# Kernel optimization log

Measured on AMD Instinct MI355X. Metric: run time of the kernel, lower is better.

The kernel has to match this reference:

```python
import jax, jax.numpy as jnp
import numpy as np

# ViT-Base config
C, H, W = 3, 224, 224
NP = 14            # n_patches per side
PS = 16            # patch size (H // NP)
IN_D = C * PS * PS # 768
D = 768            # hidden_d
NH = 12            # n_heads
DH = D // NH       # 64
L = 12             # n_blocks
MLP = 4 * D        # mlp_ratio * hidden_d
OUT = 1000         # out_d
B = 64             # batch
S = NP * NP + 1    # 197 tokens (cls + patches)
EPS = 1e-5


def _pos_embed(seq_len, d):
    # get_positional_embeddings: sin on even dims, cos on odd dims
    i = jnp.arange(seq_len, dtype=jnp.float32)[:, None]
    j = jnp.arange(d, dtype=jnp.float32)[None, :]
    angle = i / jnp.power(10000.0, (j - j % 2) / d)
    return jnp.where(j % 2 == 0, jnp.sin(angle), jnp.cos(angle))


def _ln(x, g, b):
    m = x.mean(-1, keepdims=True)
    v = ((x - m) ** 2).mean(-1, keepdims=True)
    return (x - m) * jax.lax.rsqrt(v + EPS) * g + b


def _attn(x, qkv_w, qkv_b, out_w, out_b):
    n, s, _ = x.shape
    qkv = (x @ qkv_w + qkv_b).reshape(n, s, NH, 3, DH)  # matches torch chunk layout
    q, k, v = qkv[..., 0, :], qkv[..., 1, :], qkv[..., 2, :]
    scores = jnp.einsum('bqhd,bkhd->bhqk', q, k) / (DH ** 0.5)
    w = jax.nn.softmax(scores, axis=-1)
    o = jnp.einsum('bhqk,bkhd->bqhd', w, v).reshape(n, s, D)
    return o @ out_w + out_b


def setup_inputs() -> dict:
    key = jax.random.key(0)
    ks = jax.random.split(key, 16)
    sd = 0.02
    return {
        'images': jax.random.normal(ks[0], (B, C, H, W), jnp.float32),
        'lm_w': jax.random.normal(ks[1], (IN_D, D), jnp.float32) * sd,
        'lm_b': jnp.zeros((D,), jnp.float32),
        'cls_tok': jax.random.uniform(ks[2], (1, D), jnp.float32),
        'ln1_g': jnp.ones((L, D), jnp.float32),
        'ln1_b': jnp.zeros((L, D), jnp.float32),
        'qkv_w': jax.random.normal(ks[3], (L, D, 3 * D), jnp.float32) * sd,
        'qkv_b': jnp.zeros((L, 3 * D), jnp.float32),
        'out_w': jax.random.normal(ks[4], (L, D, D), jnp.float32) * sd,
        'out_b': jnp.zeros((L, D), jnp.float32),
        'ln2_g': jnp.ones((L, D), jnp.float32),
        'ln2_b': jnp.zeros((L, D), jnp.float32),
        'mlp1_w': jax.random.normal(ks[5], (L, D, MLP), jnp.float32) * sd,
        'mlp1_b': jnp.zeros((L, MLP), jnp.float32),
        'mlp2_w': jax.random.normal(ks[6], (L, MLP, D), jnp.float32) * sd,
        'mlp2_b': jnp.zeros((L, D), jnp.float32),
        'head_w': jax.random.normal(ks[7], (D, OUT), jnp.float32) * sd,
        'head_b': jnp.zeros((OUT,), jnp.float32),
    }


def reference(images, lm_w, lm_b, cls_tok, ln1_g, ln1_b, qkv_w, qkv_b,
              out_w, out_b, ln2_g, ln2_b, mlp1_w, mlp1_b, mlp2_w, mlp2_b,
              head_w, head_b):
    n = images.shape[0]
    # patchify: (N,C,H,W) -> (N, NP*NP, C*PS*PS), per-patch flatten order (C, ph, pw)
    p = images.reshape(n, C, NP, PS, NP, PS).transpose(0, 2, 4, 1, 3, 5)
    p = p.reshape(n, NP * NP, IN_D)
    tok = p @ lm_w + lm_b                                   # (N, 196, D)
    cls = jnp.broadcast_to(cls_tok, (n, 1, D))
    x = jnp.concatenate([cls, tok], axis=1) + _pos_embed(S, D)
    for l in range(L):
        x = x + _attn(_ln(x, ln1_g[l], ln1_b[l]), qkv_w[l], qkv_b[l], out_w[l], out_b[l])
        h = _ln(x, ln2_g[l], ln2_b[l])
        x = x + (jax.nn.gelu(h @ mlp1_w[l] + mlp1_b[l], approximate=False) @ mlp2_w[l] + mlp2_b[l])
    return jax.nn.softmax(x[:, 0] @ head_w + head_b, axis=-1)
```

## Files before the change

### kernel.cpp

```cpp
#include <hip/hip_runtime.h>
#include <hip/hip_bf16.h>
#include <math.h>

#define WS_B 64
#define WS_S 197
#define WS_D 768
#define WS_NH 12
#define WS_L 12
#define WS_MLP 3072
#define WS_OUT 1000
#define WS_IND 768
#define WS_NPAT 196
#define SP 208
#define JP 224

typedef __attribute__((ext_vector_type(8))) short bf16x8;
typedef __attribute__((ext_vector_type(4))) float f32x4;

static __device__ __forceinline__ float bf2f(short s) {
    unsigned u = ((unsigned)(unsigned short)s) << 16;
    return __builtin_bit_cast(float, u);
}
static __device__ __forceinline__ short f2bf(float f) {
    unsigned u = __builtin_bit_cast(unsigned, f);
    u = (u + 0x7FFF + ((u >> 16) & 1)) >> 16;
    return (short)u;
}

__global__ __launch_bounds__(256) void wconv_kernel(
    const float* __restrict__ W, short* __restrict__ Wh, int K, int N)
{
    int idx = blockIdx.x * 256 + threadIdx.x;
    int total = (K >> 3) * N;
    if (idx >= total) return;
    int n = idx % N, k8 = idx / N, k0 = k8 << 3;
    short hi[8];
#pragma unroll
    for (int j = 0; j < 8; ++j) hi[j] = f2bf(W[(size_t)(k0 + j) * N + n]);
    *(bf16x8*)(Wh + (size_t)n * K + k0) = *(bf16x8*)hi;
}

__global__ __launch_bounds__(256) void mfma_gemm(
    const short* __restrict__ A, int lda,
    const short* __restrict__ Bh,
    const float* __restrict__ bias, const float* __restrict__ res,
    float* __restrict__ outF, short* __restrict__ outH, int ldc,
    int M, int N, int K, int act)
{
    __shared__ short As[128 * 64];
    __shared__ short Bs[128 * 64];

    const int tid = threadIdx.x;
    const int w = tid >> 6, lane = tid & 63;
    const int bm = blockIdx.y * 128, bn = blockIdx.x * 128;
    const int wm = (w >> 1) * 64, wn = (w & 1) * 64;
    const int lr = lane & 15, lq = lane >> 4;

    f32x4 acc[4][4];
#pragma unroll
    for (int i = 0; i < 4; ++i)
#pragma unroll
        for (int j = 0; j < 4; ++j) acc[i][j] = (f32x4){0.f, 0.f, 0.f, 0.f};

    int aoff[2][4], boff[2][4];
#pragma unroll
    for (int ks = 0; ks < 2; ++ks)
#pragma unroll
        for (int f = 0; f < 4; ++f) {
            int r = wm + f * 16 + lr;
            aoff[ks][f] = r * 64 + (((ks * 4 + lq) ^ (lr & 7)) << 3);
            int rn = wn + f * 16 + lr;
            boff[ks][f] = rn * 64 + (((ks * 4 + lq) ^ (lr & 7)) << 3);
        }

    int srow[4], scs[4];
#pragma unroll
    for (int i = 0; i < 4; ++i) {
        int chunk = w * 64 + i * 256 + lane;
        int row = chunk >> 3, c = chunk & 7;
        srow[i] = row;
        scs[i] = c ^ (row & 7);
    }

    for (int k0 = 0; k0 < K; k0 += 64) {
#pragma unroll
        for (int i = 0; i < 4; ++i) {
            int ldsbase = (w * 64 + i * 256) * 8;
            int arow = bm + srow[i]; if (arow >= M) arow = M - 1;
            const short* ga = A + (size_t)arow * lda + k0 + scs[i] * 8;
            __builtin_amdgcn_global_load_lds(
                (const __attribute__((address_space(1))) void*)ga,
                (__attribute__((address_space(3))) void*)(As + ldsbase), 16, 0, 0);
            const short* gh = Bh + (size_t)(bn + srow[i]) * K + k0 + scs[i] * 8;
            __builtin_amdgcn_global_load_lds(
                (const __attribute__((address_space(1))) void*)gh,
                (__attribute__((address_space(3))) void*)(Bs + ldsbase), 16, 0, 0);
        }
        asm volatile("s_waitcnt vmcnt(0)" ::: "memory");
        __syncthreads();

#pragma unroll
        for (int ks = 0; ks < 2; ++ks) {
            bf16x8 av[4], bv[4];
#pragma unroll
            for (int f = 0; f < 4; ++f) av[f] = *(const bf16x8*)&As[aoff[ks][f]];
#pragma unroll
            for (int f = 0; f < 4; ++f) bv[f] = *(const bf16x8*)&Bs[boff[ks][f]];
#pragma unroll
            for (int fm = 0; fm < 4; ++fm)
#pragma unroll
                for (int fn = 0; fn < 4; ++fn)
                    acc[fm][fn] = __builtin_amdgcn_mfma_f32_16x16x32_bf16(
                        av[fm], bv[fn], acc[fm][fn], 0, 0, 0);
        }
        __syncthreads();
    }

#pragma unroll
    for (int fm = 0; fm < 4; ++fm)
#pragma unroll
        for (int fn = 0; fn < 4; ++fn) {
            int gc = bn + wn + fn * 16 + lr;
            float bvs = bias ? bias[gc] : 0.f;
            int grb = bm + wm + fm * 16 + lq * 4;
#pragma unroll
            for (int r = 0; r < 4; ++r) {
                int gr = grb + r;
                if (gr >= M) continue;
                float v = acc[fm][fn][r] + bvs;
                if (act == 1) v = 0.5f * v * (1.f + erff(v * 0.70710678118654752440f));
                if (res) v += res[(size_t)gr * ldc + gc];
                if (outF) outF[(size_t)gr * ldc + gc] = v;
                else      outH[(size_t)gr * ldc + gc] = f2bf(v);
            }
        }
}

__global__ __launch_bounds__(256) void attn_kernel(
    const short* __restrict__ qkv, short* __restrict__ o)
{
    __shared__ short Qs[SP * 64];
    __shared__ short Ks[SP * 64];
    __shared__ short Vt[64 * 256];
    __shared__ short Ps[4][16 * 256];

    const int bh = blockIdx.x;
    const int n = bh / WS_NH, h = bh % WS_NH;
    const short* base = qkv + (size_t)n * WS_S * 2304 + h * 192;
    const int tid = threadIdx.x;
    const int w = tid >> 6, lane = tid & 63;
    const int lr = lane & 15, lq = lane >> 4;

    const bf16x8 z8 = {0, 0, 0, 0, 0, 0, 0, 0};
    for (int i = lane; i < 512; i += 64) *(bf16x8*)&Ps[w][i * 8] = z8;

    for (int u = tid; u < SP * 8; u += 256) {
        int row = u >> 3, c = u & 7;
        int cs = c ^ (row & 7);
        bf16x8 vq = z8, vk = z8;
        if (row < WS_S) {
            const short* rp = base + (size_t)row * 2304;
            vq = *(const bf16x8*)(rp + cs * 8);
            vk = *(const bf16x8*)(rp + 64 + cs * 8);
        }
        *(bf16x8*)&Qs[row * 64 + c * 8] = vq;
        *(bf16x8*)&Ks[row * 64 + c * 8] = vk;
    }

    for (int u = tid; u < 64 * (JP / 2); u += 256) {
        int d = u & 63, jp = u >> 6;
        int j = jp * 2;
        unsigned val = 0;
        if (j < WS_S) {
            unsigned lo = (unsigned short)base[(size_t)j * 2304 + 128 + d];
            unsigned hi = (j + 1 < WS_S) ? (unsigned short)base[(size_t)(j + 1) * 2304 + 128 + d] : 0u;
            val = lo | (hi << 16);
        }
        int cj = j >> 3, e = j & 7;
        *(unsigned*)&Vt[d * 256 + ((cj ^ (d & 7)) << 3) + e] = val;
    }
    __syncthreads();

    for (int qt = w; qt < 13; qt += 4) {
        bf16x8 qv[2];
#pragma unroll
        for (int ks = 0; ks < 2; ++ks)
            qv[ks] = *(const bf16x8*)&Qs[(qt * 16 + lr) * 64 + (((ks * 4 + lq) ^ (lr & 7)) << 3)];
        f32x4 acc[13];
#pragma unroll
        for (int jt = 0; jt < 13; ++jt) acc[jt] = (f32x4){0.f, 0.f, 0.f, 0.f};
#pragma unroll
        for (int jt = 0; jt < 13; ++jt)
#pragma unroll
            for (int ks = 0; ks < 2; ++ks) {
                bf16x8 kv = *(const bf16x8*)&Ks[(jt * 16 + lr) * 64 + (((ks * 4 + lq) ^ (lr & 7)) << 3)];
                acc[jt] = __builtin_amdgcn_mfma_f32_16x16x32_bf16(kv, qv[ks], acc[jt], 0, 0, 0);
            }

        float s[13][4];
        float m = -1e30f;
#pragma unroll
        for (int jt = 0; jt < 13; ++jt)
#pragma unroll
            for (int r = 0; r < 4; ++r) {
                int j = jt * 16 + lq * 4 + r;
                float v = acc[jt][r] * 0.125f;
                s[jt][r] = v;
                if (j < WS_S) m = fmaxf(m, v);
            }
        m = fmaxf(m, __shfl_xor(m, 16));
        m = fmaxf(m, __shfl_xor(m, 32));
        float sum = 0.f;
#pragma unroll
        for (int jt = 0; jt < 13; ++jt)
#pragma unroll
            for (int r = 0; r < 4; ++r) {
                int j = jt * 16 + lq * 4 + r;
                float e = (j < WS_S) ? __expf(s[jt][r] - m) : 0.f;
                s[jt][r] = e;
                sum += e;
            }
        sum += __shfl_xor(sum, 16);
        sum += __shfl_xor(sum, 32);
        float inv = (sum > 0.f) ? 1.f / sum : 0.f;

#pragma unroll
        for (int jt = 0; jt < 13; ++jt) {
            int jb = jt * 16 + lq * 4;
            int cj = jb >> 3, e = jb & 7;
            int off = lr * 256 + ((cj ^ (lr & 7)) << 3) + e;
            unsigned p01 = (unsigned)(unsigned short)f2bf(s[jt][0] * inv) |
                           ((unsigned)(unsigned short)f2bf(s[jt][1] * inv) << 16);
            unsigned p23 = (unsigned)(unsigned short)f2bf(s[jt][2] * inv) |
                           ((unsigned)(unsigned short)f2bf(s[jt][3] * inv) << 16);
            *(unsigned*)&Ps[w][off] = p01;
            *(unsigned*)&Ps[w][off + 2] = p23;
        }

        bf16x8 pa[7];
#pragma unroll
        for (int ks = 0; ks < 7; ++ks)
            pa[ks] = *(const bf16x8*)&Ps[w][lr * 256 + (((ks * 4 + lq) ^ (lr & 7)) << 3)];
#pragma unroll
        for (int dt = 0; dt < 4; ++dt) {
            f32x4 oacc = (f32x4){0.f, 0.f, 0.f, 0.f};
#pragma unroll
            for (int ks = 0; ks < 7; ++ks) {
                bf16x8 vb = *(const bf16x8*)&Vt[(dt * 16 + lr) * 256 + (((ks * 4 + lq) ^ (lr & 7)) << 3)];
                oacc = __builtin_amdgcn_mfma_f32_16x16x32_bf16(pa[ks], vb, oacc, 0, 0, 0);
            }
#pragma unroll
            for (int r = 0; r < 4; ++r) {
                int qg = qt * 16 + lq * 4 + r;
                if (qg < WS_S)
                    o[((size_t)n * WS_S + qg) * WS_D + h * 64 + dt * 16 + lr] = f2bf(oacc[r]);
            }
        }
    }
}

__global__ __launch_bounds__(256) void gemm_kernel(
    const float* __restrict__ A, int lda,
    const float* __restrict__ B, int ldb,
    const float* __restrict__ bias,
    float* __restrict__ C, int ldc,
    int M, int N, int K)
{
    __shared__ float As[16][128];
    __shared__ float Bs[16][128];
    const int tid = threadIdx.x;
    const int tx = tid & 15, ty = tid >> 4;
    const int bm = blockIdx.y * 128, bn = blockIdx.x * 128;
    float acc[8][8];
#pragma unroll
    for (int i = 0; i < 8; ++i)
#pragma unroll
        for (int j = 0; j < 8; ++j) acc[i][j] = 0.f;
    const int arow = tid >> 2, acol4 = (tid & 3) << 2;
    const int brow = tid >> 5, bcol4 = (tid & 31) << 2;
    for (int k0 = 0; k0 < K; k0 += 16) {
#pragma unroll
        for (int r = 0; r < 2; ++r) {
            int m = bm + arow + r * 64;
            int k = k0 + acol4;
            float4 v = make_float4(0.f, 0.f, 0.f, 0.f);
            if (m < M) {
                const float* ap = A + (size_t)m * lda + k;
                if (k + 3 < K) v = *(const float4*)ap;
                else { if (k < K) v.x = ap[0]; if (k + 1 < K) v.y = ap[1]; if (k + 2 < K) v.z = ap[2]; }
            }
            As[acol4 + 0][arow + r * 64] = v.x;
            As[acol4 + 1][arow + r * 64] = v.y;
            As[acol4 + 2][arow + r * 64] = v.z;
            As[acol4 + 3][arow + r * 64] = v.w;
        }
#pragma unroll
        for (int r = 0; r < 2; ++r) {
            int k = k0 + brow + r * 8;
            int nn = bn + bcol4;
            float4 v = make_float4(0.f, 0.f, 0.f, 0.f);
            if (k < K) {
                const float* bp = B + (size_t)k * ldb + nn;
                if (nn + 3 < N) v = *(const float4*)bp;
                else { if (nn < N) v.x = bp[0]; if (nn + 1 < N) v.y = bp[1]; if (nn + 2 < N) v.z = bp[2]; }
            }
            *(float4*)&Bs[brow + r * 8][bcol4] = v;
        }
        __syncthreads();
#pragma unroll
        for (int kk = 0; kk < 16; ++kk) {
            float4 a0 = *(const float4*)&As[kk][ty * 4];
            float4 a1 = *(const float4*)&As[kk][64 + ty * 4];
            float4 b0 = *(const float4*)&Bs[kk][tx * 4];
            float4 b1 = *(const float4*)&Bs[kk][64 + tx * 4];
            float a[8] = {a0.x, a0.y, a0.z, a0.w, a1.x, a1.y, a1.z, a1.w};
            float b[8] = {b0.x, b0.y, b0.z, b0.w, b1.x, b1.y, b1.z, b1.w};
#pragma unroll
            for (int i = 0; i < 8; ++i)
#pragma unroll
                for (int j = 0; j < 8; ++j) acc[i][j] += a[i] * b[j];
        }
        __syncthreads();
    }
#pragma unroll
    for (int i = 0; i < 8; ++i) {
        int m = bm + ((i < 4) ? (ty * 4 + i) : (64 + ty * 4 + i - 4));
        if (m >= M) continue;
#pragma unroll
        for (int j = 0; j < 8; ++j) {
            int nn = bn + ((j < 4) ? (tx * 4 + j) : (64 + tx * 4 + j - 4));
            if (nn >= N) continue;
            C[(size_t)m * ldc + nn] = acc[i][j] + (bias ? bias[nn] : 0.f);
        }
    }
}

__global__ __launch_bounds__(256) void ln_kernel(
    const float* __restrict__ x, const float* __restrict__ g,
    const float* __restrict__ b, short* __restrict__ y)
{
    __shared__ float ssum[4], ssq[4];
    const int row = blockIdx.x;
    const int tid = threadIdx.x;
    const float* xr = x + (size_t)row * WS_D;
    float v0 = xr[tid], v1 = xr[tid + 256], v2 = xr[tid + 512];
    float s = v0 + v1 + v2;
    float q = v0 * v0 + v1 * v1 + v2 * v2;
#pragma unroll
    for (int off = 32; off > 0; off >>= 1) {
        s += __shfl_xor(s, off);
        q += __shfl_xor(q, off);
    }
    if ((tid & 63) == 0) { ssum[tid >> 6] = s; ssq[tid >> 6] = q; }
    __syncthreads();
    s = ssum[0] + ssum[1] + ssum[2] + ssum[3];
    q = ssq[0] + ssq[1] + ssq[2] + ssq[3];
    const float mean = s * (1.f / WS_D);
    const float var = q * (1.f / WS_D) - mean * mean;
    const float rstd = rsqrtf(var + 1e-5f);
    short* yr = y + (size_t)row * WS_D;
    yr[tid]       = f2bf((v0 - mean) * rstd * g[tid]       + b[tid]);
    yr[tid + 256] = f2bf((v1 - mean) * rstd * g[tid + 256] + b[tid + 256]);
    yr[tid + 512] = f2bf((v2 - mean) * rstd * g[tid + 512] + b[tid + 512]);
}

__global__ void pe_kernel(float* __restrict__ pe)
{
    int idx = blockIdx.x * 256 + threadIdx.x;
    if (idx >= WS_S * WS_D) return;
    int s = idx / WS_D, j = idx % WS_D;
    float expo = (float)(j & ~1) / (float)WS_D;
    float angle = (float)s * powf(10000.f, -expo);
    pe[idx] = (j & 1) ? cosf(angle) : sinf(angle);
}

__global__ void patchify_kernel(const float* __restrict__ img, short* __restrict__ p)
{
    int idx = blockIdx.x * 256 + threadIdx.x;
    const int total = WS_B * WS_NPAT * WS_IND;
    if (idx >= total) return;
    int pid = idx / WS_IND;
    int e = idx % WS_IND;
    int n = pid / WS_NPAT, patch = pid % WS_NPAT;
    int c = e >> 8, r = e & 255;
    int iy = r >> 4, ix = r & 15;
    int py = patch / 14, px = patch % 14;
    p[idx] = f2bf(img[(((size_t)n * 3 + c) * 224 + py * 16 + iy) * 224 + px * 16 + ix]);
}

__global__ void assemble_kernel(const float* __restrict__ tok, const float* __restrict__ cls,
                                const float* __restrict__ pe, float* __restrict__ x)
{
    int idx = blockIdx.x * 256 + threadIdx.x;
    const int total = WS_B * WS_S * WS_D;
    if (idx >= total) return;
    int row = idx / WS_D, d = idx % WS_D;
    int n = row / WS_S, s = row % WS_S;
    float v = (s == 0) ? cls[d] : tok[((size_t)n * WS_NPAT + (s - 1)) * WS_D + d];
    x[idx] = v + pe[s * WS_D + d];
}

__global__ __launch_bounds__(256) void softmax1000_kernel(
    const float* __restrict__ logits, float* __restrict__ out)
{
    __shared__ float rmax[4], rsum[4];
    const int row = blockIdx.x;
    const int tid = threadIdx.x;
    const float* lr = logits + (size_t)row * WS_OUT;
    float v[4];
    float mx = -INFINITY;
#pragma unroll
    for (int i = 0; i < 4; ++i) {
        int c = tid + i * 256;
        v[i] = (c < WS_OUT) ? lr[c] : -INFINITY;
        mx = fmaxf(mx, v[i]);
    }
#pragma unroll
    for (int off = 32; off > 0; off >>= 1) mx = fmaxf(mx, __shfl_xor(mx, off));
    if ((tid & 63) == 0) rmax[tid >> 6] = mx;
    __syncthreads();
    mx = fmaxf(fmaxf(rmax[0], rmax[1]), fmaxf(rmax[2], rmax[3]));
    float sum = 0.f;
#pragma unroll
    for (int i = 0; i < 4; ++i) {
        int c = tid + i * 256;
        v[i] = (c < WS_OUT) ? expf(v[i] - mx) : 0.f;
        sum += v[i];
    }
#pragma unroll
    for (int off = 32; off > 0; off >>= 1) sum += __shfl_xor(sum, off);
    if ((tid & 63) == 0) rsum[tid >> 6] = sum;
    __syncthreads();
    sum = rsum[0] + rsum[1] + rsum[2] + rsum[3];
    const float inv = 1.f / sum;
#pragma unroll
    for (int i = 0; i < 4; ++i) {
        int c = tid + i * 256;
        if (c < WS_OUT) out[(size_t)row * WS_OUT + c] = v[i] * inv;
    }
}

extern "C" void kernel_launch(void* const* d_in, const int* in_sizes, int n_in,
                              void* d_out, int out_size, void* d_ws, size_t ws_size,
                              hipStream_t stream)
{
    const float* images = (const float*)d_in[0];
    const float* lm_w   = (const float*)d_in[1];
    const float* lm_b   = (const float*)d_in[2];
    const float* cls    = (const float*)d_in[3];
    const float* ln1_g  = (const float*)d_in[4];
    const float* ln1_b  = (const float*)d_in[5];
    const float* qkv_w  = (const float*)d_in[6];
    const float* qkv_b  = (const float*)d_in[7];
    const float* out_w  = (const float*)d_in[8];
    const float* out_b  = (const float*)d_in[9];
    const float* ln2_g  = (const float*)d_in[10];
    const float* ln2_b  = (const float*)d_in[11];
    const float* mlp1_w = (const float*)d_in[12];
    const float* mlp1_b = (const float*)d_in[13];
    const float* mlp2_w = (const float*)d_in[14];
    const float* mlp2_b = (const float*)d_in[15];
    const float* head_w = (const float*)d_in[16];
    const float* head_b = (const float*)d_in[17];

    const int ROWS = WS_B * WS_S;
    char* wsb = (char*)d_ws;
    size_t off = 0;
    auto alloc = [&](size_t bytes) {
        void* p = wsb + off;
        off += (bytes + 255) & ~(size_t)255;
        return p;
    };
    float* pe     = (float*)alloc((size_t)WS_S * WS_D * 4);
    float* x      = (float*)alloc((size_t)ROWS * WS_D * 4);
    short* xh     = (short*)alloc((size_t)ROWS * WS_D * 2);
    short* qkvh   = (short*)alloc((size_t)ROWS * 2304 * 2);
    short* oh     = (short*)alloc((size_t)ROWS * WS_D * 2);
    short* hh     = (short*)alloc((size_t)ROWS * WS_MLP * 2);
    float* logits = (float*)alloc((size_t)WS_B * WS_OUT * 4);
    short* ph     = (short*)alloc((size_t)WS_B * WS_NPAT * WS_IND * 2);
    short* qWh  = (short*)alloc((size_t)WS_D * 2304 * 2);
    short* oWh  = (short*)alloc((size_t)WS_D * WS_D * 2);
    short* m1Wh = (short*)alloc((size_t)WS_D * WS_MLP * 2);
    short* m2Wh = (short*)alloc((size_t)WS_MLP * WS_D * 2);
    short* lmWh = (short*)alloc((size_t)WS_IND * WS_D * 2);
    float* tok  = (float*)hh;

    pe_kernel<<<(WS_S * WS_D + 255) / 256, 256, 0, stream>>>(pe);
    patchify_kernel<<<(WS_B * WS_NPAT * WS_IND + 255) / 256, 256, 0, stream>>>(images, ph);
    wconv_kernel<<<(WS_IND / 8 * WS_D + 255) / 256, 256, 0, stream>>>(lm_w, lmWh, WS_IND, WS_D);
    mfma_gemm<<<dim3(6, 98), 256, 0, stream>>>(
        ph, WS_IND, lmWh, lm_b, nullptr, tok, nullptr, WS_D,
        WS_B * WS_NPAT, WS_D, WS_IND, 0);
    assemble_kernel<<<(WS_B * WS_S * WS_D + 255) / 256, 256, 0, stream>>>(tok, cls, pe, x);

    for (int l = 0; l < WS_L; ++l) {
        wconv_kernel<<<(WS_D / 8 * 2304 + 255) / 256, 256, 0, stream>>>(
            qkv_w + (size_t)l * WS_D * 2304, qWh, WS_D, 2304);
        wconv_kernel<<<(WS_D / 8 * WS_D + 255) / 256, 256, 0, stream>>>(
            out_w + (size_t)l * WS_D * WS_D, oWh, WS_D, WS_D);
        wconv_kernel<<<(WS_D / 8 * WS_MLP + 255) / 256, 256, 0, stream>>>(
            mlp1_w + (size_t)l * WS_D * WS_MLP, m1Wh, WS_D, WS_MLP);
        wconv_kernel<<<(WS_MLP / 8 * WS_D + 255) / 256, 256, 0, stream>>>(
            mlp2_w + (size_t)l * WS_MLP * WS_D, m2Wh, WS_MLP, WS_D);

        ln_kernel<<<ROWS, 256, 0, stream>>>(x, ln1_g + l * WS_D, ln1_b + l * WS_D, xh);
        mfma_gemm<<<dim3(18, 99), 256, 0, stream>>>(
            xh, WS_D, qWh, qkv_b + l * 2304, nullptr, nullptr, qkvh, 2304,
            ROWS, 2304, WS_D, 0);
        attn_kernel<<<WS_B * WS_NH, 256, 0, stream>>>(qkvh, oh);
        mfma_gemm<<<dim3(6, 99), 256, 0, stream>>>(
            oh, WS_D, oWh, out_b + l * WS_D, x, x, nullptr, WS_D,
            ROWS, WS_D, WS_D, 0);
        ln_kernel<<<ROWS, 256, 0, stream>>>(x, ln2_g + l * WS_D, ln2_b + l * WS_D, xh);
        mfma_gemm<<<dim3(24, 99), 256, 0, stream>>>(
            xh, WS_D, m1Wh, mlp1_b + l * WS_MLP, nullptr, nullptr, hh, WS_MLP,
            ROWS, WS_MLP, WS_D, 1);
        mfma_gemm<<<dim3(6, 99), 256, 0, stream>>>(
            hh, WS_MLP, m2Wh, mlp2_b + l * WS_D, x, x, nullptr, WS_D,
            ROWS, WS_D, WS_MLP, 0);
    }

    gemm_kernel<<<dim3(8, 1), 256, 0, stream>>>(
        x, WS_S * WS_D, head_w, WS_OUT, head_b, logits, WS_OUT,
        WS_B, WS_OUT, WS_D);
    softmax1000_kernel<<<WS_B, 256, 0, stream>>>(logits, (float*)d_out);
}
```

Measured before the change: 6.266 ms.

## Use 256x256 double-buffered MFMA GEMM with 512 threads and simpler head kernel

Replaces the 128x128 single-buffered bf16 MFMA GEMM with a 256x256 tile, 512-thread kernel that double-buffers LDS (128 KB), so the next K-tile's global-to-LDS loads are issued before computing on the current one. It also uses s_setprio around the MFMA bursts and per-row swizzle fix. The fp32 tiled head GEMM is replaced by a simple per-thread dot-product kernel, and a waitcnt is added in attention. Larger tiles raise data reuse but halve grid size (fewer blocks for 12.6k rows, e.g. 150 blocks for N=768), risking low occupancy and wave quantization on a 256-CU part.

Result: slower. 7.528 ms (+20.1%).

```diff
diff --git a/kernel.cpp b/kernel.cpp
--- a/kernel.cpp
+++ b/kernel.cpp
@@ -40,84 +40,112 @@
     *(bf16x8*)(Wh + (size_t)n * K + k0) = *(bf16x8*)hi;
 }
 
-__global__ __launch_bounds__(256) void mfma_gemm(
+__global__ __launch_bounds__(512) void gemm2(
     const short* __restrict__ A, int lda,
     const short* __restrict__ Bh,
     const float* __restrict__ bias, const float* __restrict__ res,
     float* __restrict__ outF, short* __restrict__ outH, int ldc,
     int M, int N, int K, int act)
 {
-    __shared__ short As[128 * 64];
-    __shared__ short Bs[128 * 64];
+    __shared__ short lds[65536];
 
     const int tid = threadIdx.x;
     const int w = tid >> 6, lane = tid & 63;
-    const int bm = blockIdx.y * 128, bn = blockIdx.x * 128;
-    const int wm = (w >> 1) * 64, wn = (w & 1) * 64;
+    const int bm = blockIdx.y * 256, bn = blockIdx.x * 256;
+    const int wm = (w >> 2) * 128, wn = (w & 3) * 64;
     const int lr = lane & 15, lq = lane >> 4;
 
-    f32x4 acc[4][4];
-#pragma unroll
-    for (int i = 0; i < 4; ++i)
+    f32x4 acc[8][4];
+#pragma unroll
+    for (int i = 0; i < 8; ++i)
 #pragma unroll
         for (int j = 0; j < 4; ++j) acc[i][j] = (f32x4){0.f, 0.f, 0.f, 0.f};
 
-    int aoff[2][4], boff[2][4];
-#pragma unroll
-    for (int ks = 0; ks < 2; ++ks)
+    int aoff[2][8], boff[2][4];
+#pragma unroll
+    for (int ks = 0; ks < 2; ++ks) {
+#pragma unroll
+        for (int f = 0; f < 8; ++f) {
+            int r = wm + f * 16 + lr;
+            aoff[ks][f] = r * 64 + (((ks * 4 + lq) ^ (r & 7)) << 3);
+        }
 #pragma unroll
         for (int f = 0; f < 4; ++f) {
-            int r = wm + f * 16 + lr;
-            aoff[ks][f] = r * 64 + (((ks * 4 + lq) ^ (lr & 7)) << 3);
-            int rn = wn + f * 16 + lr;
-            boff[ks][f] = rn * 64 + (((ks * 4 + lq) ^ (lr & 7)) << 3);
-        }
+            int r = wn + f * 16 + lr;
+            boff[ks][f] = r * 64 + (((ks * 4 + lq) ^ (r & 7)) << 3);
+        }
+    }
 
     int srow[4], scs[4];
 #pragma unroll
     for (int i = 0; i < 4; ++i) {
-        int chunk = w * 64 + i * 256 + lane;
-        int row = chunk >> 3, c = chunk & 7;
+        int cid = i * 512 + tid;
+        int row = cid >> 3, c = cid & 7;
         srow[i] = row;
         scs[i] = c ^ (row & 7);
     }
 
-    for (int k0 = 0; k0 < K; k0 += 64) {
+    const int nt = K >> 6;
+
+    auto STAGE = [&](int kt, int slot) {
+        const int k0 = kt << 6;
+        short* Ab = &lds[slot * 16384];
+        short* Bb = &lds[32768 + slot * 16384];
 #pragma unroll
         for (int i = 0; i < 4; ++i) {
-            int ldsbase = (w * 64 + i * 256) * 8;
+            int cid = i * 512 + tid;
             int arow = bm + srow[i]; if (arow >= M) arow = M - 1;
             const short* ga = A + (size_t)arow * lda + k0 + scs[i] * 8;
             __builtin_amdgcn_global_load_lds(
                 (const __attribute__((address_space(1))) void*)ga,
-                (__attribute__((address_space(3))) void*)(As + ldsbase), 16, 0, 0);
-            const short* gh = Bh + (size_t)(bn + srow[i]) * K + k0 + scs[i] * 8;
+                (__attribute__((address_space(3))) void*)(Ab + cid * 8), 16, 0, 0);
+            const short* gb = Bh + (size_t)(bn + srow[i]) * K + k0 + scs[i] * 8;
             __builtin_amdgcn_global_load_lds(
-                (const __attribute__((address_space(1))) void*)gh,
-                (__attribute__((address_space(3))) void*)(Bs + ldsbase), 16, 0, 0);
-        }
-        asm volatile("s_waitcnt vmcnt(0)" ::: "memory");
-        __syncthreads();
-
+                (const __attribute__((address_space(1))) void*)gb,
+                (__attribute__((address_space(3))) void*)(Bb + cid * 8), 16, 0, 0);
+        }
+    };
+
+    STAGE(0, 0);
+
+    for (int t = 0; t < nt; ++t) {
+        if (t + 1 < nt) {
+            STAGE(t + 1, (t + 1) & 1);
+            asm volatile("s_waitcnt vmcnt(8)" ::: "memory");
+        } else {
+            asm volatile("s_waitcnt vmcnt(0)" ::: "memory");
+        }
+        __builtin_amdgcn_s_barrier();
+        asm volatile("" ::: "memory");
+
+        const short* Ab = &lds[(t & 1) * 16384];
+        const short* Bb = &lds[32768 + (t & 1) * 16384];
 #pragma unroll
         for (int ks = 0; ks < 2; ++ks) {
-            bf16x8 av[4], bv[4];
-#pragma unroll
-            for (int f = 0; f < 4; ++f) av[f] = *(const bf16x8*)&As[aoff[ks][f]];
-#pragma unroll
-            for (int f = 0; f < 4; ++f) bv[f] = *(const bf16x8*)&Bs[boff[ks][f]];
-#pragma unroll
-            for (int fm = 0; fm < 4; ++fm)
-#pragma unroll
-                for (int fn = 0; fn < 4; ++fn)
-                    acc[fm][fn] = __builtin_amdgcn_mfma_f32_16x16x32_bf16(
-                        av[fm], bv[fn], acc[fm][fn], 0, 0, 0);
-        }
-        __syncthreads();
-    }
-
-#pragma unroll
-    for (int fm = 0; fm < 4; ++fm)
+            bf16x8 av[8];
+#pragma unroll
+            for (int f = 0; f < 8; ++f) av[f] = *(const bf16x8*)&Ab[aoff[ks][f]];
+#pragma unroll
+            for (int nh = 0; nh < 2; ++nh) {
+                bf16x8 bv0 = *(const bf16x8*)&Bb[boff[ks][nh * 2]];
+                bf16x8 bv1 = *(const bf16x8*)&Bb[boff[ks][nh * 2 + 1]];
+                __builtin_amdgcn_s_setprio(1);
+#pragma unroll
+                for (int fm = 0; fm < 8; ++fm) {
+                    acc[fm][nh * 2]     = __builtin_amdgcn_mfma_f32_16x16x32_bf16(
+                        av[fm], bv0, acc[fm][nh * 2], 0, 0, 0);
+                    acc[fm][nh * 2 + 1] = __builtin_amdgcn_mfma_f32_16x16x32_bf16(
+                        av[fm], bv1, acc[fm][nh * 2 + 1], 0, 0, 0);
+                }
+                __builtin_amdgcn_s_setprio(0);
+                __builtin_amdgcn_s_barrier();
+                asm volatile("" ::: "memory");
+            }
+        }
+    }
+
+#pragma unroll
+    for (int fm = 0; fm < 8; ++fm)
 #pragma unroll
         for (int fn = 0; fn < 4; ++fn) {
             int gc = bn + wn + fn * 16 + lr;
@@ -236,6 +264,7 @@
             *(unsigned*)&Ps[w][off] = p01;
             *(unsigned*)&Ps[w][off + 2] = p23;
         }
+        __builtin_amdgcn_s_waitcnt(0);
 
         bf16x8 pa[7];
 #pragma unroll
@@ -259,80 +288,18 @@
     }
 }
 
-__global__ __launch_bounds__(256) void gemm_kernel(
-    const float* __restrict__ A, int lda,
-    const float* __restrict__ B, int ldb,
-    const float* __restrict__ bias,
-    float* __restrict__ C, int ldc,
-    int M, int N, int K)
-{
-    __shared__ float As[16][128];
-    __shared__ float Bs[16][128];
-    const int tid = threadIdx.x;
-    const int tx = tid & 15, ty = tid >> 4;
-    const int bm = blockIdx.y * 128, bn = blockIdx.x * 128;
-    float acc[8][8];
-#pragma unroll
-    for (int i = 0; i < 8; ++i)
-#pragma unroll
-        for (int j = 0; j < 8; ++j) acc[i][j] = 0.f;
-    const int arow = tid >> 2, acol4 = (tid & 3) << 2;
-    const int brow = tid >> 5, bcol4 = (tid & 31) << 2;
-    for (int k0 = 0; k0 < K; k0 += 16) {
-#pragma unroll
-        for (int r = 0; r < 2; ++r) {
-            int m = bm + arow + r * 64;
-            int k = k0 + acol4;
-            float4 v = make_float4(0.f, 0.f, 0.f, 0.f);
-            if (m < M) {
-                const float* ap = A + (size_t)m * lda + k;
-                if (k + 3 < K) v = *(const float4*)ap;
-                else { if (k < K) v.x = ap[0]; if (k + 1 < K) v.y = ap[1]; if (k + 2 < K) v.z = ap[2]; }
-            }
-            As[acol4 + 0][arow + r * 64] = v.x;
-            As[acol4 + 1][arow + r * 64] = v.y;
-            As[acol4 + 2][arow + r * 64] = v.z;
-            As[acol4 + 3][arow + r * 64] = v.w;
-        }
-#pragma unroll
-        for (int r = 0; r < 2; ++r) {
-            int k = k0 + brow + r * 8;
-            int nn = bn + bcol4;
-            float4 v = make_float4(0.f, 0.f, 0.f, 0.f);
-            if (k < K) {
-                const float* bp = B + (size_t)k * ldb + nn;
-                if (nn + 3 < N) v = *(const float4*)bp;
-                else { if (nn < N) v.x = bp[0]; if (nn + 1 < N) v.y = bp[1]; if (nn + 2 < N) v.z = bp[2]; }
-            }
-            *(float4*)&Bs[brow + r * 8][bcol4] = v;
-        }
-        __syncthreads();
-#pragma unroll
-        for (int kk = 0; kk < 16; ++kk) {
-            float4 a0 = *(const float4*)&As[kk][ty * 4];
-            float4 a1 = *(const float4*)&As[kk][64 + ty * 4];
-            float4 b0 = *(const float4*)&Bs[kk][tx * 4];
-            float4 b1 = *(const float4*)&Bs[kk][64 + tx * 4];
-            float a[8] = {a0.x, a0.y, a0.z, a0.w, a1.x, a1.y, a1.z, a1.w};
-            float b[8] = {b0.x, b0.y, b0.z, b0.w, b1.x, b1.y, b1.z, b1.w};
-#pragma unroll
-            for (int i = 0; i < 8; ++i)
-#pragma unroll
-                for (int j = 0; j < 8; ++j) acc[i][j] += a[i] * b[j];
-        }
-        __syncthreads();
-    }
-#pragma unroll
-    for (int i = 0; i < 8; ++i) {
-        int m = bm + ((i < 4) ? (ty * 4 + i) : (64 + ty * 4 + i - 4));
-        if (m >= M) continue;
-#pragma unroll
-        for (int j = 0; j < 8; ++j) {
-            int nn = bn + ((j < 4) ? (tx * 4 + j) : (64 + tx * 4 + j - 4));
-            if (nn >= N) continue;
-            C[(size_t)m * ldc + nn] = acc[i][j] + (bias ? bias[nn] : 0.f);
-        }
-    }
+__global__ __launch_bounds__(256) void head_kernel(
+    const float* __restrict__ x, const float* __restrict__ W,
+    const float* __restrict__ bias, float* __restrict__ out)
+{
+    int c = blockIdx.x * 16 + (threadIdx.x & 15);
+    int m = blockIdx.y * 16 + (threadIdx.x >> 4);
+    if (c >= WS_OUT) return;
+    const float* xr = x + (size_t)m * (WS_S * WS_D);
+    float acc = bias[c];
+    for (int k = 0; k < WS_D; ++k)
+        acc = fmaf(xr[k], W[(size_t)k * WS_OUT + c], acc);
+    out[(size_t)m * WS_OUT + c] = acc;
 }
 
 __global__ __launch_bounds__(256) void ln_kernel(
@@ -489,7 +456,7 @@
     pe_kernel<<<(WS_S * WS_D + 255) / 256, 256, 0, stream>>>(pe);
     patchify_kernel<<<(WS_B * WS_NPAT * WS_IND + 255) / 256, 256, 0, stream>>>(images, ph);
     wconv_kernel<<<(WS_IND / 8 * WS_D + 255) / 256, 256, 0, stream>>>(lm_w, lmWh, WS_IND, WS_D);
-    mfma_gemm<<<dim3(6, 98), 256, 0, stream>>>(
+    gemm2<<<dim3(3, 49), 512, 0, stream>>>(
         ph, WS_IND, lmWh, lm_b, nullptr, tok, nullptr, WS_D,
         WS_B * WS_NPAT, WS_D, WS_IND, 0);
     assemble_kernel<<<(WS_B * WS_S * WS_D + 255) / 256, 256, 0, stream>>>(tok, cls, pe, x);
@@ -505,24 +472,22 @@
             mlp2_w + (size_t)l * WS_MLP * WS_D, m2Wh, WS_MLP, WS_D);
 
         ln_kernel<<<ROWS, 256, 0, stream>>>(x, ln1_g + l * WS_D, ln1_b + l * WS_D, xh);
-        mfma_gemm<<<dim3(18, 99), 256, 0, stream>>>(
+        gemm2<<<dim3(9, 50), 512, 0, stream>>>(
             xh, WS_D, qWh, qkv_b + l * 2304, nullptr, nullptr, qkvh, 2304,
             ROWS, 2304, WS_D, 0);
         attn_kernel<<<WS_B * WS_NH, 256, 0, stream>>>(qkvh, oh);
-        mfma_gemm<<<dim3(6, 99), 256, 0, stream>>>(
+        gemm2<<<dim3(3, 50), 512, 0, stream>>>(
             oh, WS_D, oWh, out_b + l * WS_D, x, x, nullptr, WS_D,
             ROWS, WS_D, WS_D, 0);
         ln_kernel<<<ROWS, 256, 0, stream>>>(x, ln2_g + l * WS_D, ln2_b + l * WS_D, xh);
-        mfma_gemm<<<dim3(24, 99), 256, 0, stream>>>(
+        gemm2<<<dim3(12, 50), 512, 0, stream>>>(
             xh, WS_D, m1Wh, mlp1_b + l * WS_MLP, nullptr, nullptr, hh, WS_MLP,
             ROWS, WS_MLP, WS_D, 1);
-        mfma_gemm<<<dim3(6, 99), 256, 0, stream>>>(
+        gemm2<<<dim3(3, 50), 512, 0, stream>>>(
             hh, WS_MLP, m2Wh, mlp2_b + l * WS_D, x, x, nullptr, WS_D,
             ROWS, WS_D, WS_MLP, 0);
     }
 
-    gemm_kernel<<<dim3(8, 1), 256, 0, stream>>>(
-        x, WS_S * WS_D, head_w, WS_OUT, head_b, logits, WS_OUT,
-        WS_B, WS_OUT, WS_D);
+    head_kernel<<<dim3((WS_OUT + 15) / 16, 4), 256, 0, stream>>>(x, head_w, head_b, logits);
     softmax1000_kernel<<<WS_B, 256, 0, stream>>>(logits, (float*)d_out);
 }
```
